# Kernel optimization log

Hardware: AMD Instinct MI355X
Metric: run time of the kernel (lower is better)

## Reference

```python
import jax, jax.numpy as jnp
import numpy as np
import math

B, S, D, H = 8, 1024, 512, 8
DH = D // H
SCALE_BASE = 512


def _xpos(x, downscale):
    # x: [B, H, S, DH]; xpos rotary with exponential scale (jamie-stirling RetNet impl)
    s = x.shape[-2]
    d = x.shape[-1]
    half = d // 2
    sv = (jnp.arange(0, d, 2, dtype=jnp.float32) + 0.4 * d) / (1.4 * d)      # [half]
    power = jnp.arange(s, dtype=jnp.float32) / SCALE_BASE
    scale = sv[None, :] ** power[:, None]                                     # [s, half]
    inv_freq = 1.0 / (10000.0 ** (jnp.arange(half, dtype=jnp.float32) / half))
    ang = jnp.arange(s, dtype=jnp.float32)[:, None] * inv_freq[None, :]       # [s, half]
    if downscale:
        scale = 1.0 / scale
    sin = jnp.repeat(jnp.sin(ang) * scale, 2, axis=-1)                        # [s, d]
    cos = jnp.repeat(jnp.cos(ang) * scale, 2, axis=-1)
    rot = jnp.stack((-x[..., 1::2], x[..., ::2]), axis=-1).reshape(x.shape)   # rotate_every_two
    return x * cos + rot * sin


def setup_inputs() -> dict:
    key = jax.random.key(0)
    ks = jax.random.split(key, 7)
    X = jax.random.normal(ks[0], (B, S, D), dtype=jnp.float32)
    # per-head projections stacked: torch init randn/hidden_size
    W_Q = jax.random.normal(ks[1], (H, D, DH), dtype=jnp.float32) / D
    W_K = jax.random.normal(ks[2], (H, D, DH), dtype=jnp.float32) / D
    W_V = jax.random.normal(ks[3], (H, D, DH), dtype=jnp.float32) / D
    W_G = jax.random.normal(ks[4], (D, D), dtype=jnp.float32) / D
    W_O = jax.random.normal(ks[5], (D, D), dtype=jnp.float32) / D
    gn_weight = jnp.ones((D,), dtype=jnp.float32)
    gn_bias = jnp.zeros((D,), dtype=jnp.float32)
    return {"X": X, "W_Q": W_Q, "W_K": W_K, "W_V": W_V, "W_G": W_G,
            "W_O": W_O, "gn_weight": gn_weight, "gn_bias": gn_bias}


def reference(X, W_Q, W_K, W_V, W_G, W_O, gn_weight, gn_bias):
    b, s, _ = X.shape
    # per-head decay gammas and symmetric (non-causal) decay matrix D
    gammas = 1.0 - jnp.exp(jnp.linspace(math.log(1.0 / 32), math.log(1.0 / 512), H)).astype(jnp.float32)
    n = jnp.arange(s)
    Dmat = gammas[:, None, None] ** jnp.abs(n[:, None] - n[None, :]).astype(jnp.float32)  # [H,s,s]
    Q = _xpos(jnp.einsum('bsd,hde->bhse', X, W_Q), False)
    K = _xpos(jnp.einsum('bsd,hde->bhse', X, W_K), True)
    V = jnp.einsum('bsd,hde->bhse', X, W_V)
    scores = jnp.einsum('bhse,bhte->bhst', Q, K)
    p = jax.nn.softmax(scores, axis=-1) * Dmat[None]          # decay-weighted softmax
    Y = jnp.einsum('bhst,bhte->bhse', p, V)                    # [b,H,s,DH]
    Y = jnp.moveaxis(Y, 1, 2).reshape(b, s, H * DH)            # concat heads -> [b,s,D]
    # GroupNorm(H groups) over flattened rows [b*s, D]
    Yg = Y.reshape(-1, H, DH)
    mu = Yg.mean(axis=-1, keepdims=True)
    var = Yg.var(axis=-1, keepdims=True)
    Yn = ((Yg - mu) * jax.lax.rsqrt(var + 1e-5)).reshape(-1, H * DH)
    Yn = (Yn * gn_weight + gn_bias).reshape(b, s, H * DH)
    G = X @ W_G
    swish = G * jax.nn.sigmoid(G)
    return (swish * Yn) @ W_O
```

## Files before the change

### kernel.cpp

```cpp
#include <hip/hip_runtime.h>
#include <math.h>

#define B_ 8
#define S_ 1024
#define D_ 512
#define H_ 8
#define DH_ 64
#define M_ (B_*S_)

typedef __attribute__((ext_vector_type(8))) short short8;
typedef __attribute__((ext_vector_type(4))) short s16x4;
typedef __attribute__((ext_vector_type(4))) float f32x4;

__device__ inline void tsplit(float x, short& hs, short& ls) {
  unsigned u = __float_as_uint(x);
  hs = (short)(u >> 16);
  float r = x - __uint_as_float(u & 0xFFFF0000u);
  ls = (short)(__float_as_uint(r) >> 16);
}
__device__ inline f32x4 mfma16(short8 a, short8 b, f32x4 c) {
  return __builtin_amdgcn_mfma_f32_16x16x32_bf16(a, b, c, 0, 0, 0);
}
__device__ inline void gload_lds16(const void* g, void* l) {
  __builtin_amdgcn_global_load_lds(
      (const __attribute__((address_space(1))) void*)g,
      (__attribute__((address_space(3))) void*)l, 16, 0, 0);
}

__global__ void xpos_table_kernel(float* __restrict__ tab) {
  int idx = blockIdx.x * 256 + threadIdx.x;
  int s = idx >> 5, i = idx & 31;
  float sv = (2.0f * (float)i + 0.4f * 64.0f) / (1.4f * 64.0f);
  float p = (float)s / 512.0f;
  float scale = powf(sv, p);
  float inv_freq = powf(10000.0f, -((float)i / 32.0f));
  float ang = (float)s * inv_freq;
  float sn = sinf(ang), cs = cosf(ang);
  tab[idx]          = cs * scale;
  tab[32768 + idx]  = sn * scale;
  tab[65536 + idx]  = cs / scale;
  tab[98304 + idx]  = sn / scale;
}

__global__ __launch_bounds__(256) void wprep_kernel(
    const float* __restrict__ Wq, const float* __restrict__ Wk,
    const float* __restrict__ Wv, const float* __restrict__ Wg,
    short* __restrict__ BTh, short* __restrict__ BTl, int gonly) {
  __shared__ float t[64][65];
  const int n0 = blockIdx.x * 64, k0 = blockIdx.y * 64;
  const int tid = threadIdx.x;
  const float* src;
  int ld;
  if (gonly) {
    src = Wg + (size_t)k0 * 512 + n0; ld = 512;
  } else {
    int w = n0 >> 9, nn = n0 & 511;
    if (w == 3) { src = Wg + (size_t)k0 * 512 + nn; ld = 512; }
    else {
      const float* W = (w == 0) ? Wq : ((w == 1) ? Wk : Wv);
      int h = nn >> 6;
      src = W + (size_t)h * D_ * DH_ + (size_t)k0 * 64; ld = 64;
    }
  }
#pragma unroll
  for (int i = 0; i < 4; ++i) {
    int idx = tid + i * 256;
    int kk = idx >> 4, nl4 = (idx & 15) * 4;
    float4 v = *(const float4*)(src + (size_t)kk * ld + nl4);
    t[kk][nl4] = v.x; t[kk][nl4 + 1] = v.y; t[kk][nl4 + 2] = v.z; t[kk][nl4 + 3] = v.w;
  }
  __syncthreads();
#pragma unroll
  for (int i = 0; i < 2; ++i) {
    int idx = tid + i * 256;
    int nl = idx >> 3, ck = idx & 7;
    short8 hh, ll;
#pragma unroll
    for (int j = 0; j < 8; ++j) {
      short h_, l_;
      tsplit(t[ck * 8 + j][nl], h_, l_);
      hh[j] = h_; ll[j] = l_;
    }
    size_t off = (size_t)(n0 + nl) * 512 + k0 + ck * 8;
    *(short8*)(BTh + off) = hh;
    *(short8*)(BTl + off) = ll;
  }
}

template<int AMODE, int NSUB>
__global__ __launch_bounds__(256) void gemm_mfma_kernel(
    const float* __restrict__ Af,
    const short* __restrict__ Ah, const short* __restrict__ Al,
    const short* __restrict__ BTh, const short* __restrict__ BTl,
    const float* __restrict__ tab,
    short* __restrict__ QhO, short* __restrict__ QlO,
    short* __restrict__ KhO, short* __restrict__ KlO,
    short* __restrict__ VhT, short* __restrict__ VlT,
    float* __restrict__ G, int fused) {
  constexpr int NT = NSUB * 32;
  constexpr int ASTR = (AMODE == 0) ? 40 : 32;
  __shared__ __align__(16) short AsH[128][ASTR];
  __shared__ __align__(16) short AsL[128][ASTR];
  __shared__ __align__(16) short BsH[NT][32];
  __shared__ __align__(16) short BsL[NT][32];
  const int m0 = blockIdx.x * 128, by = blockIdx.y, n0 = by * NT;
  const int tid = threadIdx.x, w = tid >> 6, lane = tid & 63;
  const int lx = lane & 15, quad = lane >> 4;
  const int wr = w >> 1, wc = w & 1;
  f32x4 acc[4][NSUB] = {};
  for (int k0 = 0; k0 < 512; k0 += 32) {
    if constexpr (AMODE == 0) {
      int r = tid >> 1, cb = (tid & 1) * 16;
      const float* ap = Af + (size_t)(m0 + r) * 512 + k0 + cb;
      short8 hh[2], ll[2];
#pragma unroll
      for (int j4 = 0; j4 < 4; ++j4) {
        float4 v = *(const float4*)(ap + j4 * 4);
        short h_, l_;
        tsplit(v.x, h_, l_); hh[j4 >> 1][(j4 & 1) * 4 + 0] = h_; ll[j4 >> 1][(j4 & 1) * 4 + 0] = l_;
        tsplit(v.y, h_, l_); hh[j4 >> 1][(j4 & 1) * 4 + 1] = h_; ll[j4 >> 1][(j4 & 1) * 4 + 1] = l_;
        tsplit(v.z, h_, l_); hh[j4 >> 1][(j4 & 1) * 4 + 2] = h_; ll[j4 >> 1][(j4 & 1) * 4 + 2] = l_;
        tsplit(v.w, h_, l_); hh[j4 >> 1][(j4 & 1) * 4 + 3] = h_; ll[j4 >> 1][(j4 & 1) * 4 + 3] = l_;
      }
      *(short8*)&AsH[r][cb]     = hh[0];
      *(short8*)&AsH[r][cb + 8] = hh[1];
      *(short8*)&AsL[r][cb]     = ll[0];
      *(short8*)&AsL[r][cb + 8] = ll[1];
    } else {
#pragma unroll
      for (int c = 0; c < 2; ++c) {
        int ch = w + c * 4;
        size_t goff = (size_t)(m0 + ch * 16 + (lane >> 2)) * 512 + k0 + (lane & 3) * 8;
        gload_lds16(Ah + goff, &AsH[ch * 16][0]);
        gload_lds16(Al + goff, &AsL[ch * 16][0]);
      }
    }
    {
      constexpr int NCH = NT / 16;
#pragma unroll
      for (int ch = 0; ch < NCH; ch += 4) {
        int c = w + ch;
        if (c < NCH) {
          size_t goff = (size_t)(n0 + c * 16 + (lane >> 2)) * 512 + k0 + (lane & 3) * 8;
          gload_lds16(BTh + goff, &BsH[c * 16][0]);
          gload_lds16(BTl + goff, &BsL[c * 16][0]);
        }
      }
    }
    __syncthreads();
    short8 fah[4], fal[4], fbh[NSUB], fbl[NSUB];
#pragma unroll
    for (int i = 0; i < 4; ++i) {
      fah[i] = *(const short8*)&AsH[wr * 64 + i * 16 + lx][quad * 8];
      fal[i] = *(const short8*)&AsL[wr * 64 + i * 16 + lx][quad * 8];
    }
#pragma unroll
    for (int i = 0; i < NSUB; ++i) {
      fbh[i] = *(const short8*)&BsH[wc * (NSUB * 16) + i * 16 + lx][quad * 8];
      fbl[i] = *(const short8*)&BsL[wc * (NSUB * 16) + i * 16 + lx][quad * 8];
    }
#pragma unroll
    for (int ms = 0; ms < 4; ++ms)
#pragma unroll
      for (int ns = 0; ns < NSUB; ++ns) {
        f32x4 a = acc[ms][ns];
        a = mfma16(fah[ms], fbh[ns], a);
        a = mfma16(fal[ms], fbh[ns], a);
        a = mfma16(fah[ms], fbl[ns], a);
        acc[ms][ns] = a;
      }
    __syncthreads();
  }
  if (fused) {
    const int w4 = by >> 2;
    const int ncb = (by & 3) * 128 + wc * 64;
    if (w4 < 2) {
      short* Ph = (w4 == 0) ? QhO : KhO;
      short* Pl = (w4 == 0) ? QlO : KlO;
      const float* ct = tab + (w4 ? 65536 : 0);
      const float* st = tab + (w4 ? 98304 : 32768);
#pragma unroll
      for (int ms = 0; ms < 4; ++ms) {
        const int m = m0 + wr * 64 + ms * 16 + quad * 4;
        const int b = m >> 10, sbase = m & 1023;
#pragma unroll
        for (int ns = 0; ns < 4; ++ns) {
          const int n = ncb + ns * 16 + lx;
          const int h = n >> 6, e = n & 63;
          const int i0 = e >> 1;
          const float sgn = (e & 1) ? 1.0f : -1.0f;
          short* ph = Ph + (((size_t)(b * 8 + h)) * 1024 + sbase) * 64 + e;
          short* pl = Pl + (((size_t)(b * 8 + h)) * 1024 + sbase) * 64 + e;
#pragma unroll
          for (int rg = 0; rg < 4; ++rg) {
            const int s = sbase + rg;
            float v = acc[ms][ns][rg];
            float vp = __shfl_xor(v, 1);
            float o = v * ct[s * 32 + i0] + sgn * vp * st[s * 32 + i0];
            short h_, l_;
            tsplit(o, h_, l_);
            ph[rg * 64] = h_;
            pl[rg * 64] = l_;
          }
        }
      }
    } else if (w4 == 2) {
#pragma unroll
      for (int ms = 0; ms < 4; ++ms) {
        const int m = m0 + wr * 64 + ms * 16 + quad * 4;
        const int b = m >> 10, s = m & 1023;
#pragma unroll
        for (int ns = 0; ns < 4; ++ns) {
          const int n = ncb + ns * 16 + lx;
          const int h = n >> 6, e = n & 63;
          s16x4 hh, ll;
#pragma unroll
          for (int rg = 0; rg < 4; ++rg) {
            short h_, l_;
            tsplit(acc[ms][ns][rg], h_, l_);
            hh[rg] = h_; ll[rg] = l_;
          }
          size_t off = (((size_t)(b * 8 + h)) * 64 + e) * 1024 + s;
          *(s16x4*)(VhT + off) = hh;
          *(s16x4*)(VlT + off) = ll;
        }
      }
    } else {
#pragma unroll
      for (int ms = 0; ms < 4; ++ms) {
        const int m = m0 + wr * 64 + ms * 16 + quad * 4;
#pragma unroll
        for (int ns = 0; ns < 4; ++ns) {
          const int n = ncb + ns * 16 + lx;
#pragma unroll
          for (int rg = 0; rg < 4; ++rg) G[(size_t)(m + rg) * 512 + n] = acc[ms][ns][rg];
        }
      }
    }
  } else {
#pragma unroll
    for (int ms = 0; ms < 4; ++ms) {
      const int m = m0 + wr * 64 + ms * 16 + quad * 4;
#pragma unroll
      for (int ns = 0; ns < NSUB; ++ns) {
        const int n = n0 + wc * (NSUB * 16) + ns * 16 + lx;
#pragma unroll
        for (int rg = 0; rg < 4; ++rg) G[(size_t)(m + rg) * 512 + n] = acc[ms][ns][rg];
      }
    }
  }
}

__global__ __launch_bounds__(256, 2) void attn_mfma_kernel(
    const short* __restrict__ Qh, const short* __restrict__ Ql,
    const short* __restrict__ Kh, const short* __restrict__ Kl,
    const short* __restrict__ VhT, const short* __restrict__ VlT,
    const float* __restrict__ Gp,
    const float* __restrict__ gnw, const float* __restrict__ gnb,
    short* __restrict__ Zh, short* __restrict__ Zl) {
  __shared__ __align__(16) short KhS[64][72];
  __shared__ __align__(16) short KlS[64][72];
  __shared__ __align__(16) short VhS[64][72];
  __shared__ __align__(16) short VlS[64][72];
  __shared__ __align__(16) short PhS[4][32][72];
  const int bh = blockIdx.x, s0 = blockIdx.y * 128;
  const int b = bh >> 3, h = bh & 7;
  const int tid = threadIdx.x;
  const int w = tid >> 6, lane = tid & 63;
  const int lx = lane & 15, quad = lane >> 4;
  const int s0w = s0 + w * 32;
  const float l0c = -3.4657359027997265f;
  const float l1c = -6.2383246250395075f;
  const float gamma = 1.0f - expf(l0c + (float)h * (l1c - l0c) / 7.0f);
  const float lg2g = log2f(gamma);
  const short* Qbh = Qh + (size_t)bh * S_ * DH_;
  const short* Qbl = Ql + (size_t)bh * S_ * DH_;
  const short* Kbh = Kh + (size_t)bh * S_ * DH_;
  const short* Kbl = Kl + (size_t)bh * S_ * DH_;
  const short* VbH = VhT + (size_t)bh * DH_ * S_;
  const short* VbL = VlT + (size_t)bh * DH_ * S_;

  float cl[4], cr[4], w4g[4], b4g[4];
#pragma unroll
  for (int ns = 0; ns < 4; ++ns) {
    cl[ns] = exp2f(lg2g * (float)(ns * 16 + lx));
    cr[ns] = exp2f(lg2g * (float)(63 - ns * 16 - lx));
    w4g[ns] = gnw[h * DH_ + ns * 16 + lx];
    b4g[ns] = gnb[h * DH_ + ns * 16 + lx];
  }

  short8 qfh[2][2], qfl[2][2];
#pragma unroll
  for (int ms = 0; ms < 2; ++ms)
#pragma unroll
    for (int kc = 0; kc < 2; ++kc) {
      size_t off = (size_t)(s0w + ms * 16 + lx) * DH_ + kc * 32 + quad * 8;
      qfh[ms][kc] = *(const short8*)(Qbh + off);
      qfl[ms][kc] = *(const short8*)(Qbl + off);
    }

  f32x4 O[2][4] = {};
  float lsum[2][4] = {};

  for (int t0 = 0; t0 < S_; t0 += 64) {
    __syncthreads();
#pragma unroll
    for (int i = 0; i < 2; ++i) {
      int slot = tid + i * 256;
      int r = slot >> 3, c8 = (slot & 7) * 8;
      *(short8*)&KhS[r][c8] = *(const short8*)(Kbh + (size_t)(t0 + r) * DH_ + c8);
      *(short8*)&KlS[r][c8] = *(const short8*)(Kbl + (size_t)(t0 + r) * DH_ + c8);
      *(short8*)&VhS[r][c8] = *(const short8*)(VbH + (size_t)r * S_ + t0 + c8);
      *(short8*)&VlS[r][c8] = *(const short8*)(VbL + (size_t)r * S_ + t0 + c8);
    }
    __syncthreads();
    f32x4 acc[2][4];
#pragma unroll
    for (int ns = 0; ns < 4; ++ns) {
      short8 kh0 = *(const short8*)&KhS[ns * 16 + lx][quad * 8];
      short8 kh1 = *(const short8*)&KhS[ns * 16 + lx][32 + quad * 8];
      short8 kl0 = *(const short8*)&KlS[ns * 16 + lx][quad * 8];
      short8 kl1 = *(const short8*)&KlS[ns * 16 + lx][32 + quad * 8];
#pragma unroll
      for (int ms = 0; ms < 2; ++ms) {
        f32x4 a = {};
        a = mfma16(qfh[ms][0], kh0, a);
        a = mfma16(qfl[ms][0], kh0, a);
        a = mfma16(qfh[ms][0], kl0, a);
        a = mfma16(qfh[ms][1], kh1, a);
        a = mfma16(qfl[ms][1], kh1, a);
        a = mfma16(qfh[ms][1], kl1, a);
        acc[ms][ns] = a;
      }
    }
    const int cse = (t0 + 63 < s0w) ? 0 : ((t0 > s0w + 31) ? 1 : 2);
#pragma unroll
    for (int ms = 0; ms < 2; ++ms)
#pragma unroll
      for (int rg = 0; rg < 4; ++rg) {
        const int rloc = ms * 16 + quad * 4 + rg;
        const int srow = s0w + rloc;
        float pe[4], p[4];
#pragma unroll
        for (int ns = 0; ns < 4; ++ns) pe[ns] = __expf(acc[ms][ns][rg]);
        lsum[ms][rg] += (pe[0] + pe[1]) + (pe[2] + pe[3]);
        if (cse == 0) {
          float rf = exp2f(lg2g * (float)(srow - t0 - 63));
#pragma unroll
          for (int ns = 0; ns < 4; ++ns) p[ns] = pe[ns] * rf * cr[ns];
        } else if (cse == 1) {
          float rf = exp2f(lg2g * (float)(t0 - srow));
#pragma unroll
          for (int ns = 0; ns < 4; ++ns) p[ns] = pe[ns] * rf * cl[ns];
        } else {
#pragma unroll
          for (int ns = 0; ns < 4; ++ns)
            p[ns] = pe[ns] * exp2f(lg2g * fabsf((float)(srow - (t0 + ns * 16 + lx))));
        }
#pragma unroll
        for (int ns = 0; ns < 4; ++ns)
          PhS[w][rloc][ns * 16 + lx] = (short)((__float_as_uint(p[ns]) + 0x8000u) >> 16);
      }
    short8 pf[2][2];
#pragma unroll
    for (int ms = 0; ms < 2; ++ms)
#pragma unroll
      for (int kc = 0; kc < 2; ++kc)
        pf[ms][kc] = *(const short8*)&PhS[w][ms * 16 + lx][kc * 32 + quad * 8];
#pragma unroll
    for (int ns = 0; ns < 4; ++ns) {
      short8 vh0 = *(const short8*)&VhS[ns * 16 + lx][quad * 8];
      short8 vh1 = *(const short8*)&VhS[ns * 16 + lx][32 + quad * 8];
      short8 vl0 = *(const short8*)&VlS[ns * 16 + lx][quad * 8];
      short8 vl1 = *(const short8*)&VlS[ns * 16 + lx][32 + quad * 8];
#pragma unroll
      for (int ms = 0; ms < 2; ++ms) {
        f32x4 o = O[ms][ns];
        o = mfma16(pf[ms][0], vh0, o);
        o = mfma16(pf[ms][0], vl0, o);
        o = mfma16(pf[ms][1], vh1, o);
        o = mfma16(pf[ms][1], vl1, o);
        O[ms][ns] = o;
      }
    }
  }
#pragma unroll
  for (int ms = 0; ms < 2; ++ms)
#pragma unroll
    for (int rg = 0; rg < 4; ++rg) {
      float s = lsum[ms][rg];
      s += __shfl_xor(s, 1);
      s += __shfl_xor(s, 2);
      s += __shfl_xor(s, 4);
      s += __shfl_xor(s, 8);
      const float inv = 1.0f / s;
      const int srow = s0w + ms * 16 + quad * 4 + rg;
      float y[4];
      float rs = 0.0f;
#pragma unroll
      for (int ns = 0; ns < 4; ++ns) { y[ns] = O[ms][ns][rg] * inv; rs += y[ns]; }
      rs += __shfl_xor(rs, 1);
      rs += __shfl_xor(rs, 2);
      rs += __shfl_xor(rs, 4);
      rs += __shfl_xor(rs, 8);
      const float mu = rs * (1.0f / 64.0f);
      float vv = 0.0f;
#pragma unroll
      for (int ns = 0; ns < 4; ++ns) { float d = y[ns] - mu; vv += d * d; }
      vv += __shfl_xor(vv, 1);
      vv += __shfl_xor(vv, 2);
      vv += __shfl_xor(vv, 4);
      vv += __shfl_xor(vv, 8);
      const float rstd = rsqrtf(vv * (1.0f / 64.0f) + 1e-5f);
      const size_t base = (size_t)(b * S_ + srow) * D_ + h * DH_;
#pragma unroll
      for (int ns = 0; ns < 4; ++ns) {
        float g = Gp[base + ns * 16 + lx];
        float sw = g / (1.0f + __expf(-g));
        float z = sw * ((y[ns] - mu) * rstd * w4g[ns] + b4g[ns]);
        short zh_, zl_;
        tsplit(z, zh_, zl_);
        Zh[base + ns * 16 + lx] = zh_;
        Zl[base + ns * 16 + lx] = zl_;
      }
    }
}

extern "C" void kernel_launch(void* const* d_in, const int* in_sizes, int n_in,
                              void* d_out, int out_size, void* d_ws, size_t ws_size,
                              hipStream_t stream) {
  const float* X   = (const float*)d_in[0];
  const float* Wq  = (const float*)d_in[1];
  const float* Wk  = (const float*)d_in[2];
  const float* Wv  = (const float*)d_in[3];
  const float* Wg  = (const float*)d_in[4];
  const float* Wo  = (const float*)d_in[5];
  const float* gnw = (const float*)d_in[6];
  const float* gnb = (const float*)d_in[7];
  float* out = (float*)d_out;
  float* ws  = (float*)d_ws;
  const size_t NB = (size_t)M_ * D_;
  float* R0 = ws;
  float* R1 = ws + NB;
  float* R2 = ws + 2 * NB;
  float* R3 = ws + 3 * NB;
  float* tab = ws + 4 * NB;
  short* BTh = (short*)R3;
  short* BTl = BTh + (size_t)2048 * 512;
  short* Qh = (short*)R0;  short* Ql = Qh + NB;
  short* Kh = (short*)R1;  short* Kl = Kh + NB;
  short* VhT = (short*)R2; short* VlT = VhT + NB;
  short* Zh = (short*)R3;  short* Zl = Zh + NB;
  short* BToh = (short*)R1;
  short* BTol = BToh + (size_t)512 * 512;

  wprep_kernel<<<dim3(32, 8), 256, 0, stream>>>(Wq, Wk, Wv, Wg, BTh, BTl, 0);
  xpos_table_kernel<<<128, 256, 0, stream>>>(tab);
  gemm_mfma_kernel<0, 4><<<dim3(64, 16), 256, 0, stream>>>(
      X, nullptr, nullptr, BTh, BTl, tab, Qh, Ql, Kh, Kl, VhT, VlT, out, 1);
  attn_mfma_kernel<<<dim3(64, 8), 256, 0, stream>>>(
      Qh, Ql, Kh, Kl, VhT, VlT, out, gnw, gnb, Zh, Zl);
  wprep_kernel<<<dim3(8, 8), 256, 0, stream>>>(nullptr, nullptr, nullptr, Wo, BToh, BTol, 1);
  gemm_mfma_kernel<1, 2><<<dim3(64, 8), 256, 0, stream>>>(
      nullptr, Zh, Zl, BToh, BTol, nullptr, nullptr, nullptr, nullptr, nullptr,
      nullptr, nullptr, out, 0);
}
```

Baseline: 229.0 us.

## Double-buffer GEMM LDS tiles with register prefetch and XOR-swizzled layout

Restructures the split-bf16 MFMA GEMM main loop to use two LDS buffers, so the next k-tile's global loads (and the fp32 A-tile register prefetch plus split) run while the current tile is computed. This drops one __syncthreads per iteration. It also replaces the padded A layout with an XOR swizzle on both A and B tiles to avoid LDS bank conflicts. The cost is doubled LDS use, which may reduce occupancy, plus more live registers for the prefetched A values.

Result: slower. 237.4 us (+3.7%).

```diff
diff --git a/kernel.cpp b/kernel.cpp
--- a/kernel.cpp
+++ b/kernel.cpp
@@ -87,7 +87,7 @@
   }
 }
 
-template<int AMODE, int NSUB>
+template<int NSUB, bool APRE>
 __global__ __launch_bounds__(256) void gemm_mfma_kernel(
     const float* __restrict__ Af,
     const short* __restrict__ Ah, const short* __restrict__ Al,
@@ -98,66 +98,85 @@
     short* __restrict__ VhT, short* __restrict__ VlT,
     float* __restrict__ G, int fused) {
   constexpr int NT = NSUB * 32;
-  constexpr int ASTR = (AMODE == 0) ? 40 : 32;
-  __shared__ __align__(16) short AsH[128][ASTR];
-  __shared__ __align__(16) short AsL[128][ASTR];
-  __shared__ __align__(16) short BsH[NT][32];
-  __shared__ __align__(16) short BsL[NT][32];
+  __shared__ __align__(16) short AsH[2][128][32];
+  __shared__ __align__(16) short AsL[2][128][32];
+  __shared__ __align__(16) short BsH[2][NT][32];
+  __shared__ __align__(16) short BsL[2][NT][32];
   const int m0 = blockIdx.x * 128, by = blockIdx.y, n0 = by * NT;
   const int tid = threadIdx.x, w = tid >> 6, lane = tid & 63;
   const int lx = lane & 15, quad = lane >> 4;
   const int wr = w >> 1, wc = w & 1;
+
+  float4 av[4];
+  auto loadA = [&](int k0) {
+    const float* ap = Af + (size_t)(m0 + (tid >> 1)) * 512 + k0 + (tid & 1) * 16;
+#pragma unroll
+    for (int j = 0; j < 4; ++j) av[j] = *(const float4*)(ap + j * 4);
+  };
+  auto writeA = [&](int bf) {
+    const int r = tid >> 1, cbase = (tid & 1) * 2, swzr = (r >> 1) & 3;
+#pragma unroll
+    for (int j = 0; j < 2; ++j) {
+      float xs[8] = {av[2*j].x, av[2*j].y, av[2*j].z, av[2*j].w,
+                     av[2*j+1].x, av[2*j+1].y, av[2*j+1].z, av[2*j+1].w};
+      short8 hh, ll;
+#pragma unroll
+      for (int q = 0; q < 8; ++q) {
+        short h_, l_;
+        tsplit(xs[q], h_, l_);
+        hh[q] = h_; ll[q] = l_;
+      }
+      const int slot = ((cbase + j) ^ swzr) * 8;
+      *(short8*)&AsH[bf][r][slot] = hh;
+      *(short8*)&AsL[bf][r][slot] = ll;
+    }
+  };
+  auto stageApre = [&](int bf, int k0) {
+#pragma unroll
+    for (int c = 0; c < 2; ++c) {
+      int ch = w * 2 + c;
+      size_t goff = (size_t)(m0 + ch * 16 + (lane >> 2)) * 512 + k0 +
+                    (((lane & 3) ^ ((lane >> 3) & 3)) * 8);
+      gload_lds16(Ah + goff, &AsH[bf][ch * 16][0]);
+      gload_lds16(Al + goff, &AsL[bf][ch * 16][0]);
+    }
+  };
+  auto stageB = [&](int bf, int k0) {
+#pragma unroll
+    for (int c = 0; c < NSUB / 2; ++c) {
+      int ch = w * (NSUB / 2) + c;
+      size_t goff = (size_t)(n0 + ch * 16 + (lane >> 2)) * 512 + k0 +
+                    (((lane & 3) ^ ((lane >> 3) & 3)) * 8);
+      gload_lds16(BTh + goff, &BsH[bf][ch * 16][0]);
+      gload_lds16(BTl + goff, &BsL[bf][ch * 16][0]);
+    }
+  };
+
   f32x4 acc[4][NSUB] = {};
-  for (int k0 = 0; k0 < 512; k0 += 32) {
-    if constexpr (AMODE == 0) {
-      int r = tid >> 1, cb = (tid & 1) * 16;
-      const float* ap = Af + (size_t)(m0 + r) * 512 + k0 + cb;
-      short8 hh[2], ll[2];
-#pragma unroll
-      for (int j4 = 0; j4 < 4; ++j4) {
-        float4 v = *(const float4*)(ap + j4 * 4);
-        short h_, l_;
-        tsplit(v.x, h_, l_); hh[j4 >> 1][(j4 & 1) * 4 + 0] = h_; ll[j4 >> 1][(j4 & 1) * 4 + 0] = l_;
-        tsplit(v.y, h_, l_); hh[j4 >> 1][(j4 & 1) * 4 + 1] = h_; ll[j4 >> 1][(j4 & 1) * 4 + 1] = l_;
-        tsplit(v.z, h_, l_); hh[j4 >> 1][(j4 & 1) * 4 + 2] = h_; ll[j4 >> 1][(j4 & 1) * 4 + 2] = l_;
-        tsplit(v.w, h_, l_); hh[j4 >> 1][(j4 & 1) * 4 + 3] = h_; ll[j4 >> 1][(j4 & 1) * 4 + 3] = l_;
-      }
-      *(short8*)&AsH[r][cb]     = hh[0];
-      *(short8*)&AsH[r][cb + 8] = hh[1];
-      *(short8*)&AsL[r][cb]     = ll[0];
-      *(short8*)&AsL[r][cb + 8] = ll[1];
-    } else {
-#pragma unroll
-      for (int c = 0; c < 2; ++c) {
-        int ch = w + c * 4;
-        size_t goff = (size_t)(m0 + ch * 16 + (lane >> 2)) * 512 + k0 + (lane & 3) * 8;
-        gload_lds16(Ah + goff, &AsH[ch * 16][0]);
-        gload_lds16(Al + goff, &AsL[ch * 16][0]);
-      }
-    }
-    {
-      constexpr int NCH = NT / 16;
-#pragma unroll
-      for (int ch = 0; ch < NCH; ch += 4) {
-        int c = w + ch;
-        if (c < NCH) {
-          size_t goff = (size_t)(n0 + c * 16 + (lane >> 2)) * 512 + k0 + (lane & 3) * 8;
-          gload_lds16(BTh + goff, &BsH[c * 16][0]);
-          gload_lds16(BTl + goff, &BsL[c * 16][0]);
-        }
-      }
-    }
+  if constexpr (APRE) stageApre(0, 0); else { loadA(0); writeA(0); }
+  stageB(0, 0);
+
+  const int swzv = (lx >> 1) & 3;
+  for (int it = 0; it < 16; ++it) {
+    const int bf = it & 1;
     __syncthreads();
+    if (it < 15) {
+      stageB(bf ^ 1, (it + 1) * 32);
+      if constexpr (APRE) stageApre(bf ^ 1, (it + 1) * 32);
+      else loadA((it + 1) * 32);
+    }
     short8 fah[4], fal[4], fbh[NSUB], fbl[NSUB];
 #pragma unroll
     for (int i = 0; i < 4; ++i) {
-      fah[i] = *(const short8*)&AsH[wr * 64 + i * 16 + lx][quad * 8];
-      fal[i] = *(const short8*)&AsL[wr * 64 + i * 16 + lx][quad * 8];
+      const int row = wr * 64 + i * 16 + lx;
+      fah[i] = *(const short8*)&AsH[bf][row][(quad ^ swzv) * 8];
+      fal[i] = *(const short8*)&AsL[bf][row][(quad ^ swzv) * 8];
     }
 #pragma unroll
     for (int i = 0; i < NSUB; ++i) {
-      fbh[i] = *(const short8*)&BsH[wc * (NSUB * 16) + i * 16 + lx][quad * 8];
-      fbl[i] = *(const short8*)&BsL[wc * (NSUB * 16) + i * 16 + lx][quad * 8];
+      const int row = wc * (NSUB * 16) + i * 16 + lx;
+      fbh[i] = *(const short8*)&BsH[bf][row][(quad ^ swzv) * 8];
+      fbl[i] = *(const short8*)&BsL[bf][row][(quad ^ swzv) * 8];
     }
 #pragma unroll
     for (int ms = 0; ms < 4; ++ms)
@@ -169,7 +188,7 @@
         a = mfma16(fah[ms], fbl[ns], a);
         acc[ms][ns] = a;
       }
-    __syncthreads();
+    if constexpr (!APRE) { if (it < 15) writeA(bf ^ 1); }
   }
   if (fused) {
     const int w4 = by >> 2;
@@ -456,12 +475,12 @@
 
   wprep_kernel<<<dim3(32, 8), 256, 0, stream>>>(Wq, Wk, Wv, Wg, BTh, BTl, 0);
   xpos_table_kernel<<<128, 256, 0, stream>>>(tab);
-  gemm_mfma_kernel<0, 4><<<dim3(64, 16), 256, 0, stream>>>(
+  gemm_mfma_kernel<4, false><<<dim3(64, 16), 256, 0, stream>>>(
       X, nullptr, nullptr, BTh, BTl, tab, Qh, Ql, Kh, Kl, VhT, VlT, out, 1);
   attn_mfma_kernel<<<dim3(64, 8), 256, 0, stream>>>(
       Qh, Ql, Kh, Kl, VhT, VlT, out, gnw, gnb, Zh, Zl);
   wprep_kernel<<<dim3(8, 8), 256, 0, stream>>>(nullptr, nullptr, nullptr, Wo, BToh, BTol, 1);
-  gemm_mfma_kernel<1, 2><<<dim3(64, 8), 256, 0, stream>>>(
+  gemm_mfma_kernel<2, true><<<dim3(64, 8), 256, 0, stream>>>(
       nullptr, Zh, Zl, BToh, BTol, nullptr, nullptr, nullptr, nullptr, nullptr,
       nullptr, nullptr, out, 0);
 }
```
